# Optimization experiments

Hardware: AMD Instinct MI355X
Metric: run time of the kernel (lower is better)

## Reference

```python
import jax, jax.numpy as jnp
import numpy as np

DIM = 512
DEPTH = 4
E = 2 ** DEPTH          # 16 experts
HID = 4 * DIM           # mult = 4
B, S = 8, 4096


def setup_inputs() -> dict:
    key = jax.random.key(0)
    ks = jax.random.split(key, 7)
    sc_in = 1.0 / np.sqrt(DIM)
    sc_hid = 1.0 / np.sqrt(HID)
    return {
        "x": jax.random.normal(ks[0], (B, S, DIM), jnp.float32),
        "Wr": jax.random.normal(ks[1], (E - 1, DIM), jnp.float32) * sc_in,
        "br": jax.random.normal(ks[2], (E - 1,), jnp.float32) * 0.01,
        "W1": jax.random.normal(ks[3], (E, DIM, HID), jnp.float32) * sc_in,
        "b1": jax.random.normal(ks[4], (E, HID), jnp.float32) * 0.01,
        "W2": jax.random.normal(ks[5], (E, HID, DIM), jnp.float32) * sc_hid,
        "b2": jax.random.normal(ks[6], (E, DIM), jnp.float32) * 0.01,
    }


def _fff_forward(x, Wr, br, W1, b1, W2, b2):
    Bb, Ss, D = x.shape
    E_ = W1.shape[0]
    depth = int(np.log2(E_))
    xf = x.reshape(-1, D)                      # [N, D]
    N = xf.shape[0]

    # Hard binary-tree routing (inference path of the torch module).
    leaf = jnp.zeros((N,), jnp.int32)
    for d in range(depth):
        off = 2 ** d - 1
        cnt = 2 ** d
        # logits for all routers at this tree level: [N, cnt]
        logits = xf @ Wr[off:off + cnt].T + br[off:off + cnt]
        sel = jnp.take_along_axis(logits, leaf[:, None], axis=1)[:, 0]
        leaf = leaf * 2 + (sel > 0).astype(jnp.int32)

    onehot = jax.nn.one_hot(leaf, E_, dtype=xf.dtype)  # [N, E]

    # Dense weighted-sum dispatch: scan over the (small, fixed) expert axis,
    # accumulating masked expert outputs. Peak extra memory is one [N, HID]
    # activation at a time.
    def body(acc, params):
        w1, bb1, w2, bb2, m = params            # m: [N]
        h = jax.nn.gelu(xf @ w1 + bb1, approximate=False)  # exact GELU (torch nn.GELU)
        y = h @ w2 + bb2
        return acc + m[:, None] * y, None

    out, _ = jax.lax.scan(body, jnp.zeros_like(xf), (W1, b1, W2, b2, onehot.T))
    return out.reshape(Bb, Ss, D)


def reference(x, Wr, br, W1, b1, W2, b2):
    return _fff_forward(x, Wr, br, W1, b1, W2, b2)
```

## Files before the change

kernel.cpp:

```cpp
#include <hip/hip_runtime.h>
#include <math.h>

#define NTOK   32768
#define DMODEL 512
#define HIDDEN 2048
#define NEXP   16
#define TM     128
#define TN     128
#define BK     64
#define MAXT   272
#define PADN   (MAXT * TM)
#define CPAD   16

typedef short bf16x8 __attribute__((ext_vector_type(8)));
typedef float f32x4  __attribute__((ext_vector_type(4)));

__device__ __forceinline__ short f2bf(float f) {
  union { float f; unsigned int u; } v; v.f = f;
  unsigned int r = v.u + 0x7FFFu + ((v.u >> 16) & 1u);
  return (short)(r >> 16);
}

__device__ __forceinline__ void gload_lds16(const void* g, void* l) {
  __builtin_amdgcn_global_load_lds(
      (const __attribute__((address_space(1))) void*)g,
      (__attribute__((address_space(3))) void*)l, 16, 0, 0);
}

__device__ __forceinline__ float gelu_f(float v) {
  const float u = v * (0.7978845608f + 0.0356774081f * v * v);
  const float au = fabsf(u);
  const float z = __expf(-2.0f * au);
  float T = (1.0f - z) / (1.0f + z);
  T = copysignf(T, u);
  return 0.5f * v * (1.0f + T);
}

__global__ void init_kernel(int* counts, int* cursors) {
  counts[threadIdx.x] = 0; cursors[threadIdx.x] = 0;
}

__global__ __launch_bounds__(256) void route_kernel(
    const float* __restrict__ x, const float* __restrict__ Wr,
    const float* __restrict__ br, short* __restrict__ xb,
    int* __restrict__ leafArr) {
  const int w = threadIdx.x >> 6, l = threadIdx.x & 63;
  const int tok = blockIdx.x * 4 + w;
  const float4* xr = (const float4*)(x + (size_t)tok * DMODEL);
  float4 a0 = xr[l * 2], a1 = xr[l * 2 + 1];

  union { bf16x8 v; short s[8]; } u;
  u.s[0] = f2bf(a0.x); u.s[1] = f2bf(a0.y); u.s[2] = f2bf(a0.z); u.s[3] = f2bf(a0.w);
  u.s[4] = f2bf(a1.x); u.s[5] = f2bf(a1.y); u.s[6] = f2bf(a1.z); u.s[7] = f2bf(a1.w);
  *((bf16x8*)(xb + (size_t)tok * DMODEL) + l) = u.v;

  int leaf = 0;
  for (int d = 0; d < 4; ++d) {
    const int node = (1 << d) - 1 + leaf;
    const float4* wr4 = (const float4*)(Wr + (size_t)node * DMODEL);
    float4 b0 = wr4[l * 2], b1v = wr4[l * 2 + 1];
    double s = (double)a0.x * (double)b0.x + (double)a0.y * (double)b0.y +
               (double)a0.z * (double)b0.z + (double)a0.w * (double)b0.w +
               (double)a1.x * (double)b1v.x + (double)a1.y * (double)b1v.y +
               (double)a1.z * (double)b1v.z + (double)a1.w * (double)b1v.w;
    for (int off = 32; off; off >>= 1) s += __shfl_xor(s, off);
    double sel = s + (double)br[node];
    leaf = leaf * 2 + (sel > 0.0 ? 1 : 0);
  }
  if (l == 0) leafArr[tok] = leaf;
}

__global__ __launch_bounds__(256) void count_kernel(
    const int* __restrict__ leafArr, int* __restrict__ counts,
    int* __restrict__ idx) {
  __shared__ int lcnt[NEXP];
  const int tid = threadIdx.x;
  if (tid < NEXP) lcnt[tid] = 0;
  __syncthreads();
  const int tok = blockIdx.x * 256 + tid;
  atomicAdd(&lcnt[leafArr[tok]], 1);
  __syncthreads();
  if (tid < NEXP && lcnt[tid]) atomicAdd(&counts[tid * CPAD], lcnt[tid]);
  for (int i = blockIdx.x * 256 + tid; i < PADN; i += gridDim.x * 256) idx[i] = 0;
}

__global__ void scan_kernel(const int* __restrict__ counts, int* poff, int* ntiles,
                            int* texp, int* tval) {
  if (threadIdx.x == 0) {
    int po = 0, nt = 0;
    for (int e = 0; e < NEXP; ++e) {
      poff[e] = po;
      const int c = counts[e * CPAD];
      const int t = (c + TM - 1) >> 7;
      for (int i = 0; i < t; ++i) {
        texp[nt] = e;
        int v = c - i * TM; if (v > TM) v = TM;
        tval[nt] = v;
        ++nt;
      }
      po += t << 7;
    }
    poff[NEXP] = po;
    *ntiles = nt;
  }
}

__global__ __launch_bounds__(256) void scatter_kernel(
    const int* __restrict__ leafArr, const int* __restrict__ poff,
    int* cursors, int* __restrict__ idx) {
  __shared__ int lcnt[NEXP], lbase[NEXP];
  const int tid = threadIdx.x;
  if (tid < NEXP) lcnt[tid] = 0;
  __syncthreads();
  const int tok = blockIdx.x * 256 + tid;
  const int e = leafArr[tok];
  const int r = atomicAdd(&lcnt[e], 1);
  __syncthreads();
  if (tid < NEXP) lbase[tid] = lcnt[tid] ? atomicAdd(&cursors[tid * CPAD], lcnt[tid]) : 0;
  __syncthreads();
  idx[poff[e] + lbase[e] + r] = tok;
}

__global__ void tconv_kernel(const float* __restrict__ src, short* __restrict__ dst,
                             int R, int C) {
  __shared__ float tile[32][33];
  const int tx = threadIdx.x, ty = threadIdx.y;
  const int c0 = blockIdx.x * 32, r0 = blockIdx.y * 32;
  const size_t eoff = (size_t)blockIdx.z * R * C;
  for (int i = 0; i < 4; ++i)
    tile[ty + i * 8][tx] = src[eoff + (size_t)(r0 + ty + i * 8) * C + c0 + tx];
  __syncthreads();
  for (int i = 0; i < 4; ++i)
    dst[eoff + (size_t)(c0 + ty + i * 8) * R + r0 + tx] = f2bf(tile[tx][ty + i * 8]);
}

__global__ __launch_bounds__(256) void gemm1_kernel(
    const short* __restrict__ Xb, const short* __restrict__ W1T,
    const float* __restrict__ b1, const int* __restrict__ idx,
    const int* __restrict__ texp, const int* __restrict__ ntiles,
    short* __restrict__ H, int g0) {
  const int lt = blockIdx.x;
  const int t = g0 + lt;
  if (t >= *ntiles) return;
  const int e = texp[t];
  const int c0 = blockIdx.y * TN;

  __shared__ short smem[TM * BK * 2];
  short* As = smem;
  short* Bs = smem + TM * BK;

  const int tid = threadIdx.x, w = tid >> 6, lane = tid & 63;
  const int q = lane >> 4, cc = lane & 15;
  const int wr = (w >> 1) * 64, wc = (w & 1) * 64;
  const int srow = lane >> 3;
  const int sk = ((lane & 7) ^ srow) * 8;

  f32x4 acc[4][4];
  const f32x4 zero = {0.f, 0.f, 0.f, 0.f};
  for (int mi = 0; mi < 4; ++mi)
    for (int ni = 0; ni < 4; ++ni) acc[mi][ni] = zero;

  for (int k0 = 0; k0 < DMODEL; k0 += BK) {
    __syncthreads();
    for (int ii = 0; ii < 4; ++ii) {
      const int i = w * 4 + ii;
      const int trow = i * 8 + srow;
      const int gt = idx[t * TM + trow];
      gload_lds16(Xb + (size_t)gt * DMODEL + k0 + sk, As + i * 512);
      const int nn = c0 + i * 8 + srow;
      gload_lds16(W1T + ((size_t)e * HIDDEN + nn) * DMODEL + k0 + sk, Bs + i * 512);
    }
    __syncthreads();
    for (int ki = 0; ki < 2; ++ki) {
      const int ch = ki * 4 + q;
      const int sw = (ch ^ (cc & 7)) << 3;
      bf16x8 af[4], bfv[4];
      for (int mi = 0; mi < 4; ++mi)
        af[mi] = *(const bf16x8*)(As + (wr + mi * 16 + cc) * BK + sw);
      for (int ni = 0; ni < 4; ++ni)
        bfv[ni] = *(const bf16x8*)(Bs + (wc + ni * 16 + cc) * BK + sw);
      for (int mi = 0; mi < 4; ++mi)
        for (int ni = 0; ni < 4; ++ni)
          acc[mi][ni] = __builtin_amdgcn_mfma_f32_16x16x32_bf16(af[mi], bfv[ni], acc[mi][ni], 0, 0, 0);
    }
  }

  __syncthreads();
  short* Cs = smem;
  for (int ni = 0; ni < 4; ++ni) {
    const int col = wc + ni * 16 + cc;
    const float bv = b1[e * HIDDEN + c0 + col];
    for (int mi = 0; mi < 4; ++mi) {
      for (int r = 0; r < 4; ++r) {
        const int row = wr + mi * 16 + q * 4 + r;
        const float v = gelu_f(acc[mi][ni][r] + bv);
        Cs[row * 128 + ((((col >> 3) ^ (row & 15)) << 3) | (col & 7))] = f2bf(v);
      }
    }
  }
  __syncthreads();
  for (int it = 0; it < 8; ++it) {
    const int lin = tid + it * 256;
    const int row = lin >> 4;
    const int s = lin & 15;
    const bf16x8 vv = *(const bf16x8*)(Cs + row * 128 + s * 8);
    const int ch = s ^ (row & 15);
    *(bf16x8*)(H + ((size_t)lt * TM + row) * HIDDEN + c0 + (ch << 3)) = vv;
  }
}

__global__ __launch_bounds__(256) void gemm2_kernel(
    const short* __restrict__ H, const short* __restrict__ W2T,
    const float* __restrict__ b2, const int* __restrict__ idx,
    const int* __restrict__ texp, const int* __restrict__ tval,
    const int* __restrict__ ntiles, float* __restrict__ out, int g0) {
  const int lt = blockIdx.x;
  const int t = g0 + lt;
  if (t >= *ntiles) return;
  const int e = texp[t];
  const int c0 = blockIdx.y * TN;

  __shared__ short smem[TM * BK * 2];
  short* As = smem;
  short* Bs = smem + TM * BK;

  const int tid = threadIdx.x, w = tid >> 6, lane = tid & 63;
  const int q = lane >> 4, cc = lane & 15;
  const int wr = (w >> 1) * 64, wc = (w & 1) * 64;
  const int srow = lane >> 3;
  const int sk = ((lane & 7) ^ srow) * 8;

  f32x4 acc[4][4];
  const f32x4 zero = {0.f, 0.f, 0.f, 0.f};
  for (int mi = 0; mi < 4; ++mi)
    for (int ni = 0; ni < 4; ++ni) acc[mi][ni] = zero;

  for (int k0 = 0; k0 < HIDDEN; k0 += BK) {
    __syncthreads();
    for (int ii = 0; ii < 4; ++ii) {
      const int i = w * 4 + ii;
      const int trow = i * 8 + srow;
      gload_lds16(H + ((size_t)lt * TM + trow) * HIDDEN + k0 + sk, As + i * 512);
      const int nn = c0 + i * 8 + srow;
      gload_lds16(W2T + ((size_t)e * DMODEL + nn) * HIDDEN + k0 + sk, Bs + i * 512);
    }
    __syncthreads();
    for (int ki = 0; ki < 2; ++ki) {
      const int ch = ki * 4 + q;
      const int sw = (ch ^ (cc & 7)) << 3;
      bf16x8 af[4], bfv[4];
      for (int mi = 0; mi < 4; ++mi)
        af[mi] = *(const bf16x8*)(As + (wr + mi * 16 + cc) * BK + sw);
      for (int ni = 0; ni < 4; ++ni)
        bfv[ni] = *(const bf16x8*)(Bs + (wc + ni * 16 + cc) * BK + sw);
      for (int mi = 0; mi < 4; ++mi)
        for (int ni = 0; ni < 4; ++ni)
          acc[mi][ni] = __builtin_amdgcn_mfma_f32_16x16x32_bf16(af[mi], bfv[ni], acc[mi][ni], 0, 0, 0);
    }
  }

  const int nv = tval[t];
  for (int ni = 0; ni < 4; ++ni) {
    const int col = c0 + wc + ni * 16 + cc;
    const float bv = b2[e * DMODEL + col];
    for (int mi = 0; mi < 4; ++mi) {
      for (int r = 0; r < 4; ++r) {
        const int row = wr + mi * 16 + q * 4 + r;
        if (row < nv) {
          const int tok = idx[t * TM + row];
          out[(size_t)tok * DMODEL + col] = acc[mi][ni][r] + bv;
        }
      }
    }
  }
}

extern "C" void kernel_launch(void* const* d_in, const int* in_sizes, int n_in,
                              void* d_out, int out_size, void* d_ws, size_t ws_size,
                              hipStream_t stream) {
  (void)in_sizes; (void)n_in; (void)out_size;
  const float* x  = (const float*)d_in[0];
  const float* Wr = (const float*)d_in[1];
  const float* br = (const float*)d_in[2];
  const float* W1 = (const float*)d_in[3];
  const float* b1 = (const float*)d_in[4];
  const float* W2 = (const float*)d_in[5];
  const float* b2 = (const float*)d_in[6];
  float* out = (float*)d_out;
  char* ws = (char*)d_ws;

  int* counts  = (int*)(ws + 0);
  int* cursors = (int*)(ws + 1024);
  int* poff    = (int*)(ws + 2048);
  int* ntiles  = (int*)(ws + 2304);
  int* texp    = (int*)(ws + 4096);
  int* tval    = (int*)(ws + 8192);
  int* leafA   = (int*)(ws + 16384);
  int* idx     = (int*)(ws + 16384 + 131072);

  const size_t MB32 = 33554432ull;
  short* Xb  = (short*)(ws + (1ull << 20));
  short* W1T = (short*)(ws + (1ull << 20) + MB32);
  short* W2T = (short*)(ws + (1ull << 20) + 2 * MB32);
  short* Hb  = (short*)(ws + (1ull << 20) + 3 * MB32);
  const size_t o_h = (1ull << 20) + 3 * MB32;
  const size_t perTile = (size_t)TM * HIDDEN * sizeof(short);

  int TPG = MAXT;
  if (ws_size < o_h + (size_t)MAXT * perTile) {
    size_t avail = ws_size > o_h ? ws_size - o_h : 0;
    TPG = (int)(avail / perTile);
    if (TPG < 1) TPG = 1;
  }
  const int ngroups = (MAXT + TPG - 1) / TPG;

  hipLaunchKernelGGL(init_kernel,    dim3(1),          dim3(256),   0, stream, counts, cursors);
  hipLaunchKernelGGL(route_kernel,   dim3(NTOK / 4),   dim3(256),   0, stream, x, Wr, br, Xb, leafA);
  hipLaunchKernelGGL(count_kernel,   dim3(NTOK / 256), dim3(256),   0, stream, leafA, counts, idx);
  hipLaunchKernelGGL(scan_kernel,    dim3(1),          dim3(64),    0, stream, counts, poff, ntiles, texp, tval);
  hipLaunchKernelGGL(scatter_kernel, dim3(NTOK / 256), dim3(256),   0, stream, leafA, poff, cursors, idx);
  hipLaunchKernelGGL(tconv_kernel,   dim3(64, 16, 16), dim3(32, 8), 0, stream, W1, W1T, DMODEL, HIDDEN);
  hipLaunchKernelGGL(tconv_kernel,   dim3(16, 64, 16), dim3(32, 8), 0, stream, W2, W2T, HIDDEN, DMODEL);

  for (int g = 0; g < ngroups; ++g) {
    hipLaunchKernelGGL(gemm1_kernel, dim3(TPG, HIDDEN / TN), dim3(256), 0, stream,
                       Xb, W1T, b1, idx, texp, ntiles, Hb, g * TPG);
    hipLaunchKernelGGL(gemm2_kernel, dim3(TPG, DMODEL / TN), dim3(256), 0, stream,
                       Hb, W2T, b2, idx, texp, tval, ntiles, out, g * TPG);
  }
}
```

Before: 587.2 us.

## Use 256x256 tiles with double-buffered LDS pipeline and block swizzle in expert GEMMs

Both expert GEMMs move from 128x128 tiles with 256 threads to 256x256 tiles with 512 threads (8 waves). The K loop is now double-buffered, so global-to-LDS loads for the next K slice are issued between MFMA phases, with s_setprio raised around the MFMA blocks. A 1-D grid with an XCD-style block swizzle replaces the 2-D grid, and the routing tile size changes to 256. The aim is to hide load latency and raise arithmetic intensity per block, at the cost of more padding per expert, more registers, and 128KB of LDS per block.

```diff
diff --git a/kernel.cpp b/kernel.cpp
--- a/kernel.cpp
+++ b/kernel.cpp
@@ -5,10 +5,8 @@
 #define DMODEL 512
 #define HIDDEN 2048
 #define NEXP   16
-#define TM     128
-#define TN     128
-#define BK     64
-#define MAXT   272
+#define TM     256
+#define MAXT   144
 #define PADN   (MAXT * TM)
 #define CPAD   16
 
@@ -91,14 +89,14 @@
     for (int e = 0; e < NEXP; ++e) {
       poff[e] = po;
       const int c = counts[e * CPAD];
-      const int t = (c + TM - 1) >> 7;
+      const int t = (c + TM - 1) >> 8;
       for (int i = 0; i < t; ++i) {
         texp[nt] = e;
         int v = c - i * TM; if (v > TM) v = TM;
         tval[nt] = v;
         ++nt;
       }
-      po += t << 7;
+      po += t << 8;
     }
     poff[NEXP] = po;
     *ntiles = nt;
@@ -134,136 +132,184 @@
     dst[eoff + (size_t)(c0 + ty + i * 8) * R + r0 + tx] = f2bf(tile[tx][ty + i * 8]);
 }
 
-__global__ __launch_bounds__(256) void gemm1_kernel(
+
+#define STA(pn, ko)                                                            \
+  { _Pragma("unroll") for (int j = 0; j < 4; ++j)                              \
+      gload_lds16(aSrc[j] + (ko), lds + ((pn) << 14) + j * 4096 + w * 512); }
+
+#define STB(pn, ko)                                                            \
+  { _Pragma("unroll") for (int j = 0; j < 4; ++j)                              \
+      gload_lds16(bSrc[j] + (ko), lds + 32768 + ((pn) << 14) + j * 4096 + w * 512); }
+
+#define PHASE(mh, ki, STAGE, POST)                                             \
+  {                                                                            \
+    bf16x8 af[4];                                                              \
+    const int sw_ = ((((ki) << 2) + q) ^ (cc & 7)) << 3;                       \
+    _Pragma("unroll")                                                          \
+    for (int m2 = 0; m2 < 4; ++m2)                                             \
+      af[m2] = *(const bf16x8*)(Ab + (wr + ((mh) * 4 + m2) * 16 + cc) * 64 + sw_); \
+    if ((mh) == 0) {                                                           \
+      _Pragma("unroll")                                                        \
+      for (int ni = 0; ni < 4; ++ni)                                           \
+        bfv[ni] = *(const bf16x8*)(Bb + (wc + ni * 16 + cc) * 64 + sw_);       \
+    }                                                                          \
+    STAGE                                                                      \
+    __builtin_amdgcn_s_barrier();                                              \
+    __builtin_amdgcn_s_setprio(1);                                             \
+    _Pragma("unroll")                                                          \
+    for (int m2 = 0; m2 < 4; ++m2) {                                           \
+      _Pragma("unroll")                                                        \
+      for (int ni = 0; ni < 4; ++ni)                                           \
+        acc[(mh) * 4 + m2][ni] = __builtin_amdgcn_mfma_f32_16x16x32_bf16(      \
+            af[m2], bfv[ni], acc[(mh) * 4 + m2][ni], 0, 0, 0);                 \
+    }                                                                          \
+    __builtin_amdgcn_s_setprio(0);                                             \
+    POST                                                                       \
+    __builtin_amdgcn_s_barrier();                                              \
+  }
+
+__global__ __launch_bounds__(512, 2) void gemm1_kernel(
     const short* __restrict__ Xb, const short* __restrict__ W1T,
     const float* __restrict__ b1, const int* __restrict__ idx,
     const int* __restrict__ texp, const int* __restrict__ ntiles,
     short* __restrict__ H, int g0) {
-  const int lt = blockIdx.x;
+  __shared__ short lds[65536];
+  const int nb = gridDim.x, bid = blockIdx.x;
+  int swz = bid;
+  if ((nb & 7) == 0) { const int cpx = nb >> 3; swz = (bid & 7) * cpx + (bid >> 3); }
+  const int lt = swz >> 3, cb = swz & 7;
   const int t = g0 + lt;
   if (t >= *ntiles) return;
   const int e = texp[t];
-  const int c0 = blockIdx.y * TN;
-
-  __shared__ short smem[TM * BK * 2];
-  short* As = smem;
-  short* Bs = smem + TM * BK;
+  const int c0 = cb * 256;
 
   const int tid = threadIdx.x, w = tid >> 6, lane = tid & 63;
   const int q = lane >> 4, cc = lane & 15;
-  const int wr = (w >> 1) * 64, wc = (w & 1) * 64;
+  const int wr = (w >> 2) * 128, wc = (w & 3) * 64;
   const int srow = lane >> 3;
-  const int sk = ((lane & 7) ^ srow) * 8;
-
-  f32x4 acc[4][4];
+  const int skel = ((lane & 7) ^ srow) * 8;
+
+  const short* aSrc[4]; const short* bSrc[4];
+#pragma unroll
+  for (int j = 0; j < 4; ++j) {
+    const int r = j * 64 + w * 8 + srow;
+    const int gt = idx[t * TM + r];
+    aSrc[j] = Xb + (size_t)gt * DMODEL + skel;
+    bSrc[j] = W1T + ((size_t)e * HIDDEN + c0 + r) * DMODEL + skel;
+  }
+
+  f32x4 acc[8][4];
   const f32x4 zero = {0.f, 0.f, 0.f, 0.f};
-  for (int mi = 0; mi < 4; ++mi)
+#pragma unroll
+  for (int mi = 0; mi < 8; ++mi)
+#pragma unroll
     for (int ni = 0; ni < 4; ++ni) acc[mi][ni] = zero;
-
-  for (int k0 = 0; k0 < DMODEL; k0 += BK) {
-    __syncthreads();
-    for (int ii = 0; ii < 4; ++ii) {
-      const int i = w * 4 + ii;
-      const int trow = i * 8 + srow;
-      const int gt = idx[t * TM + trow];
-      gload_lds16(Xb + (size_t)gt * DMODEL + k0 + sk, As + i * 512);
-      const int nn = c0 + i * 8 + srow;
-      gload_lds16(W1T + ((size_t)e * HIDDEN + nn) * DMODEL + k0 + sk, Bs + i * 512);
-    }
-    __syncthreads();
-    for (int ki = 0; ki < 2; ++ki) {
-      const int ch = ki * 4 + q;
-      const int sw = (ch ^ (cc & 7)) << 3;
-      bf16x8 af[4], bfv[4];
-      for (int mi = 0; mi < 4; ++mi)
-        af[mi] = *(const bf16x8*)(As + (wr + mi * 16 + cc) * BK + sw);
-      for (int ni = 0; ni < 4; ++ni)
-        bfv[ni] = *(const bf16x8*)(Bs + (wc + ni * 16 + cc) * BK + sw);
-      for (int mi = 0; mi < 4; ++mi)
-        for (int ni = 0; ni < 4; ++ni)
-          acc[mi][ni] = __builtin_amdgcn_mfma_f32_16x16x32_bf16(af[mi], bfv[ni], acc[mi][ni], 0, 0, 0);
-    }
-  }
-
-  __syncthreads();
-  short* Cs = smem;
+  bf16x8 bfv[4];
+
+  STA(0, 0) STB(0, 0)
+  asm volatile("s_waitcnt vmcnt(0)" ::: "memory");
+  __builtin_amdgcn_s_barrier();
+
+  for (int kt = 0; kt < DMODEL / 64; ++kt) {
+    const short* Ab = lds + ((kt & 1) << 14);
+    const short* Bb = lds + 32768 + ((kt & 1) << 14);
+    const int pn = (kt & 1) ^ 1;
+    const int ko = (kt + 1) << 6;
+    const bool pre = kt < DMODEL / 64 - 1;
+    PHASE(0, 0, if (pre) STA(pn, ko), )
+    PHASE(1, 0, if (pre) STB(pn, ko), )
+    PHASE(0, 1, , )
+    PHASE(1, 1, , asm volatile("s_waitcnt vmcnt(0)" ::: "memory");)
+  }
+
+  short* Cs = lds;
+#pragma unroll
   for (int ni = 0; ni < 4; ++ni) {
     const int col = wc + ni * 16 + cc;
     const float bv = b1[e * HIDDEN + c0 + col];
-    for (int mi = 0; mi < 4; ++mi) {
+#pragma unroll
+    for (int mi = 0; mi < 8; ++mi) {
+#pragma unroll
       for (int r = 0; r < 4; ++r) {
         const int row = wr + mi * 16 + q * 4 + r;
         const float v = gelu_f(acc[mi][ni][r] + bv);
-        Cs[row * 128 + ((((col >> 3) ^ (row & 15)) << 3) | (col & 7))] = f2bf(v);
+        Cs[row * 256 + ((((col >> 3) ^ (row & 15)) << 3) | (col & 7))] = f2bf(v);
       }
     }
   }
   __syncthreads();
-  for (int it = 0; it < 8; ++it) {
-    const int lin = tid + it * 256;
-    const int row = lin >> 4;
-    const int s = lin & 15;
-    const bf16x8 vv = *(const bf16x8*)(Cs + row * 128 + s * 8);
+#pragma unroll
+  for (int it = 0; it < 16; ++it) {
+    const int lin = tid + it * 512;
+    const int row = lin >> 5;
+    const int s = lin & 31;
+    const bf16x8 vv = *(const bf16x8*)(Cs + row * 256 + s * 8);
     const int ch = s ^ (row & 15);
     *(bf16x8*)(H + ((size_t)lt * TM + row) * HIDDEN + c0 + (ch << 3)) = vv;
   }
 }
 
-__global__ __launch_bounds__(256) void gemm2_kernel(
+__global__ __launch_bounds__(512, 2) void gemm2_kernel(
     const short* __restrict__ H, const short* __restrict__ W2T,
     const float* __restrict__ b2, const int* __restrict__ idx,
     const int* __restrict__ texp, const int* __restrict__ tval,
     const int* __restrict__ ntiles, float* __restrict__ out, int g0) {
-  const int lt = blockIdx.x;
+  __shared__ short lds[65536];
+  const int nb = gridDim.x, bid = blockIdx.x;
+  int swz = bid;
+  if ((nb & 7) == 0) { const int cpx = nb >> 3; swz = (bid & 7) * cpx + (bid >> 3); }
+  const int lt = swz >> 1, cb = swz & 1;
   const int t = g0 + lt;
   if (t >= *ntiles) return;
   const int e = texp[t];
-  const int c0 = blockIdx.y * TN;
-
-  __shared__ short smem[TM * BK * 2];
-  short* As = smem;
-  short* Bs = smem + TM * BK;
+  const int c0 = cb * 256;
 
   const int tid = threadIdx.x, w = tid >> 6, lane = tid & 63;
   const int q = lane >> 4, cc = lane & 15;
-  const int wr = (w >> 1) * 64, wc = (w & 1) * 64;
+  const int wr = (w >> 2) * 128, wc = (w & 3) * 64;
   const int srow = lane >> 3;
-  const int sk = ((lane & 7) ^ srow) * 8;
-
-  f32x4 acc[4][4];
+  const int skel = ((lane & 7) ^ srow) * 8;
+
+  const short* aSrc[4]; const short* bSrc[4];
+#pragma unroll
+  for (int j = 0; j < 4; ++j) {
+    const int r = j * 64 + w * 8 + srow;
+    aSrc[j] = H + ((size_t)lt * TM + r) * HIDDEN + skel;
+    bSrc[j] = W2T + ((size_t)e * DMODEL + c0 + r) * HIDDEN + skel;
+  }
+
+  f32x4 acc[8][4];
   const f32x4 zero = {0.f, 0.f, 0.f, 0.f};
-  for (int mi = 0; mi < 4; ++mi)
+#pragma unroll
+  for (int mi = 0; mi < 8; ++mi)
+#pragma unroll
     for (int ni = 0; ni < 4; ++ni) acc[mi][ni] = zero;
-
-  for (int k0 = 0; k0 < HIDDEN; k0 += BK) {
-    __syncthreads();
-    for (int ii = 0; ii < 4; ++ii) {
-      const int i = w * 4 + ii;
-      const int trow = i * 8 + srow;
-      gload_lds16(H + ((size_t)lt * TM + trow) * HIDDEN + k0 + sk, As + i * 512);
-      const int nn = c0 + i * 8 + srow;
-      gload_lds16(W2T + ((size_t)e * DMODEL + nn) * HIDDEN + k0 + sk, Bs + i * 512);
-    }
-    __syncthreads();
-    for (int ki = 0; ki < 2; ++ki) {
-      const int ch = ki * 4 + q;
-      const int sw = (ch ^ (cc & 7)) << 3;
-      bf16x8 af[4], bfv[4];
-      for (int mi = 0; mi < 4; ++mi)
-        af[mi] = *(const bf16x8*)(As + (wr + mi * 16 + cc) * BK + sw);
-      for (int ni = 0; ni < 4; ++ni)
-        bfv[ni] = *(const bf16x8*)(Bs + (wc + ni * 16 + cc) * BK + sw);
-      for (int mi = 0; mi < 4; ++mi)
-        for (int ni = 0; ni < 4; ++ni)
-          acc[mi][ni] = __builtin_amdgcn_mfma_f32_16x16x32_bf16(af[mi], bfv[ni], acc[mi][ni], 0, 0, 0);
-    }
+  bf16x8 bfv[4];
+
+  STA(0, 0) STB(0, 0)
+  asm volatile("s_waitcnt vmcnt(0)" ::: "memory");
+  __builtin_amdgcn_s_barrier();
+
+  for (int kt = 0; kt < HIDDEN / 64; ++kt) {
+    const short* Ab = lds + ((kt & 1) << 14);
+    const short* Bb = lds + 32768 + ((kt & 1) << 14);
+    const int pn = (kt & 1) ^ 1;
+    const int ko = (kt + 1) << 6;
+    const bool pre = kt < HIDDEN / 64 - 1;
+    PHASE(0, 0, if (pre) STA(pn, ko), )
+    PHASE(1, 0, if (pre) STB(pn, ko), )
+    PHASE(0, 1, , )
+    PHASE(1, 1, , asm volatile("s_waitcnt vmcnt(0)" ::: "memory");)
   }
 
   const int nv = tval[t];
+#pragma unroll
   for (int ni = 0; ni < 4; ++ni) {
     const int col = c0 + wc + ni * 16 + cc;
     const float bv = b2[e * DMODEL + col];
-    for (int mi = 0; mi < 4; ++mi) {
+#pragma unroll
+    for (int mi = 0; mi < 8; ++mi) {
+#pragma unroll
       for (int r = 0; r < 4; ++r) {
         const int row = wr + mi * 16 + q * 4 + r;
         if (row < nv) {
@@ -310,7 +356,8 @@
   if (ws_size < o_h + (size_t)MAXT * perTile) {
     size_t avail = ws_size > o_h ? ws_size - o_h : 0;
     TPG = (int)(avail / perTile);
-    if (TPG < 1) TPG = 1;
+    TPG &= ~3;
+    if (TPG < 4) TPG = 4;
   }
   const int ngroups = (MAXT + TPG - 1) / TPG;
 
@@ -323,9 +370,9 @@
   hipLaunchKernelGGL(tconv_kernel,   dim3(16, 64, 16), dim3(32, 8), 0, stream, W2, W2T, HIDDEN, DMODEL);
 
   for (int g = 0; g < ngroups; ++g) {
-    hipLaunchKernelGGL(gemm1_kernel, dim3(TPG, HIDDEN / TN), dim3(256), 0, stream,
+    hipLaunchKernelGGL(gemm1_kernel, dim3(TPG * 8), dim3(512), 0, stream,
                        Xb, W1T, b1, idx, texp, ntiles, Hb, g * TPG);
-    hipLaunchKernelGGL(gemm2_kernel, dim3(TPG, DMODEL / TN), dim3(256), 0, stream,
+    hipLaunchKernelGGL(gemm2_kernel, dim3(TPG * 2), dim3(512), 0, stream,
                        Hb, W2T, b2, idx, texp, tval, ntiles, out, g * TPG);
   }
 }
```

Measured after the change: 572.6 us. 2.5% less time.
